# Kernel tuning notes

Measured on AMD Instinct MI355X. Metric: run time of the kernel, lower is better.

The kernel has to match this reference:

```python
import jax, jax.numpy as jnp
import numpy as np

B, S, D, H = 2, 2048, 1024, 16
HD = D // H
LOCAL_WINDOW = 32
GLOBAL_TOKENS = 16
BLOCK_SIZE = 64
SPARSITY = 0.75


def _structured_mask(seq_len):
    """local_global | block_sparse pattern, vectorized numpy (deterministic)."""
    i = np.arange(seq_len)[:, None]
    j = np.arange(seq_len)[None, :]
    half = LOCAL_WINDOW // 2
    local = np.abs(i - j) <= half  # mask[i, i-16 : i+17]
    glob = (i < GLOBAL_TOKENS) | (j < GLOBAL_TOKENS)
    stride = max(1, seq_len // 64)
    strided = ((i % stride) == 0) & ((j % stride) == 0)
    lg = local | glob | strided
    # block sparse: random blocks kept with prob 1-SPARSITY, diagonal always kept
    nb = (seq_len + BLOCK_SIZE - 1) // BLOCK_SIZE
    rng = np.random.default_rng(0)
    block_mask = rng.random((nb, nb)) > SPARSITY
    np.fill_diagonal(block_mask, True)
    bs = np.kron(block_mask, np.ones((BLOCK_SIZE, BLOCK_SIZE), dtype=bool))[:seq_len, :seq_len]
    return lg | bs


def setup_inputs() -> dict:
    key = jax.random.key(0)
    ks = jax.random.split(key, 12)
    std = 1.0 / np.sqrt(D)
    inp = {
        'query': jax.random.normal(ks[0], (B, S, D), jnp.float32),
        'key': jax.random.normal(ks[1], (B, S, D), jnp.float32),
        'value': jax.random.normal(ks[2], (B, S, D), jnp.float32),
        'Wq': jax.random.normal(ks[3], (D, D), jnp.float32) * std,
        'bq': jnp.zeros((D,), jnp.float32),
        'Wk': jax.random.normal(ks[4], (D, D), jnp.float32) * std,
        'bk': jnp.zeros((D,), jnp.float32),
        'Wv': jax.random.normal(ks[5], (D, D), jnp.float32) * std,
        'bv': jnp.zeros((D,), jnp.float32),
        'Wo': jax.random.normal(ks[6], (D, D), jnp.float32) * std,
        'bo': jnp.zeros((D,), jnp.float32),
        'sparse_mask': jnp.asarray(_structured_mask(S)),
    }
    return inp


def reference(query, key, value, Wq, bq, Wk, bk, Wv, bv, Wo, bo, sparse_mask):
    scale = HD ** -0.5
    # projections -> [B, H, S, HD]
    q = (query @ Wq + bq).reshape(B, S, H, HD).transpose(0, 2, 1, 3)
    k = (key @ Wk + bk).reshape(B, S, H, HD).transpose(0, 2, 1, 3)
    v = (value @ Wv + bv).reshape(B, S, H, HD).transpose(0, 2, 1, 3)
    # dense scores then structured sparse mask (matches original math)
    scores = jnp.einsum('bhqd,bhkd->bhqk', q, k) * scale
    scores = jnp.where(sparse_mask[None, None], scores, -jnp.inf)
    attn = jax.nn.softmax(scores, axis=-1)  # every row has >=1 active entry (global cols)
    out = jnp.einsum('bhqk,bhkd->bhqd', attn, v)
    out = out.transpose(0, 2, 1, 3).reshape(B, S, D)
    out = out @ Wo + bo
    return out, attn
```

## Files before the change

### kernel.cpp

```cpp
#include <hip/hip_runtime.h>
#include <hip/hip_bf16.h>
#include <hip/hip_fp16.h>

using u16 = unsigned short;
using u32 = unsigned int;
using u64 = unsigned long long;

typedef __attribute__((ext_vector_type(8))) short short8;
typedef __attribute__((ext_vector_type(8))) _Float16 half8;
typedef __attribute__((ext_vector_type(4))) _Float16 half4;
typedef __attribute__((ext_vector_type(4))) float f32x4;
typedef __attribute__((ext_vector_type(2))) u32 u32x2;

#define DEVI static __device__ __forceinline__

DEVI float bfu2f(u16 u) { return __builtin_bit_cast(float, (u32)u << 16); }
DEVI u16 f2bfu(float f) { return __builtin_bit_cast(u16, __float2bfloat16(f)); }
DEVI u16 f2hu(float f) { return __builtin_bit_cast(u16, (_Float16)f); }

DEVI f32x4 mfma_f16_(half8 a, half8 b, f32x4 c) {
  return __builtin_amdgcn_mfma_f32_16x16x32_f16(a, b, c, 0, 0, 0);
}
DEVI f32x4 mfma16_f16_(half4 a, half4 b, f32x4 c) {
  return __builtin_amdgcn_mfma_f32_16x16x16f16(a, b, c, 0, 0, 0);
}

#define GLD_LDS16(src, dst) \
  __builtin_amdgcn_global_load_lds((const __attribute__((address_space(1))) void*)(src), \
                                   (__attribute__((address_space(3))) void*)(dst), 16, 0, 0)

static constexpr int Bsz = 2, S = 2048, D = 1024, H = 16, HD = 64;
static constexpr int MROWS = Bsz * S;
static constexpr size_t OUT_ELEMS = (size_t)Bsz * S * D;
static constexpr float C_EXP2 = 0.18033688f;
static constexpr size_t OFF_WT  = 0;
static constexpr size_t OFF_Q   = 0x800000;
static constexpr size_t OFF_K   = 0x1000000;
static constexpr size_t OFF_V   = 0x1800000;
static constexpr size_t OFF_VT  = 0x2000000;
static constexpr size_t OFF_O   = 0x2800000;
static constexpr size_t OFF_MB  = 0x3000000;
static constexpr size_t OFF_FLG = 0x3080000;

__global__ __launch_bounds__(256) void detect_dtype(
    const u16* __restrict__ q, int* __restrict__ flag)
{
  __shared__ u32 red[256];
  const int tid = threadIdx.x;
  u32 mx = 0;
  for (int i = tid; i < 32768; i += 256) {
    u32 e = (q[2 * i] >> 7) & 0xFF;
    mx = mx > e ? mx : e;
  }
  red[tid] = mx;
  __syncthreads();
  if (tid == 0) {
    u32 m = 0;
    for (int i = 0; i < 256; ++i) m = m > red[i] ? m : red[i];
    flag[0] = (m >= 0x90) ? 1 : 0;
  }
}

__global__ __launch_bounds__(256) void conv_f16(
    const void* __restrict__ X, u16* __restrict__ Y, const int* __restrict__ flag)
{
  const size_t i8 = ((size_t)blockIdx.x * 256 + threadIdx.x) * 8;
  half8 o;
  if (*flag) {
    const float* x = (const float*)X + i8;
    float4 f0 = ((const float4*)x)[0], f1 = ((const float4*)x)[1];
    o[0] = (_Float16)f0.x; o[1] = (_Float16)f0.y;
    o[2] = (_Float16)f0.z; o[3] = (_Float16)f0.w;
    o[4] = (_Float16)f1.x; o[5] = (_Float16)f1.y;
    o[6] = (_Float16)f1.z; o[7] = (_Float16)f1.w;
  } else {
    uint4 a = *(const uint4*)((const u16*)X + i8);
    u32 wd[4] = {a.x, a.y, a.z, a.w};
    #pragma unroll
    for (int j = 0; j < 4; ++j) {
      o[2 * j]     = (_Float16)bfu2f((u16)(wd[j] & 0xFFFF));
      o[2 * j + 1] = (_Float16)bfu2f((u16)(wd[j] >> 16));
    }
  }
  *reinterpret_cast<half8*>(Y + i8) = o;
}

__global__ __launch_bounds__(256) void prep_w(
    const void* __restrict__ Wq, const void* __restrict__ Wk,
    const void* __restrict__ Wv, const void* __restrict__ Wo,
    u16* __restrict__ WT, const int* __restrict__ flag)
{
  __shared__ _Float16 t[64][80];
  const int z = blockIdx.z;
  const void* src = z == 0 ? Wq : z == 1 ? Wk : z == 2 ? Wv : Wo;
  u16* dst = WT + (size_t)z * 1024 * 1024;
  const int bx = blockIdx.x, by = blockIdx.y;
  const int tid = threadIdx.x;
  const int r = tid >> 2, ch = tid & 3;
  const int fl = *flag;
  if (fl) {
    const float* s = (const float*)src + (size_t)(by * 64 + r) * 1024 + bx * 64 + ch * 16;
    #pragma unroll
    for (int v = 0; v < 4; ++v) {
      float4 f = ((const float4*)s)[v];
      t[r][ch * 16 + v * 4 + 0] = (_Float16)f.x;
      t[r][ch * 16 + v * 4 + 1] = (_Float16)f.y;
      t[r][ch * 16 + v * 4 + 2] = (_Float16)f.z;
      t[r][ch * 16 + v * 4 + 3] = (_Float16)f.w;
    }
  } else {
    const u16* s = (const u16*)src + (size_t)(by * 64 + r) * 1024 + bx * 64 + ch * 16;
    uint4 a0 = ((const uint4*)s)[0], a1 = ((const uint4*)s)[1];
    u32 wds[8] = {a0.x, a0.y, a0.z, a0.w, a1.x, a1.y, a1.z, a1.w};
    #pragma unroll
    for (int j = 0; j < 8; ++j) {
      t[r][ch * 16 + 2 * j]     = (_Float16)bfu2f((u16)(wds[j] & 0xFFFF));
      t[r][ch * 16 + 2 * j + 1] = (_Float16)bfu2f((u16)(wds[j] >> 16));
    }
  }
  __syncthreads();
  half8 o0, o1;
  #pragma unroll
  for (int i = 0; i < 8; ++i) { o0[i] = t[ch * 16 + i][r]; o1[i] = t[ch * 16 + 8 + i][r]; }
  u16* d = dst + (size_t)(bx * 64 + r) * 1024 + by * 64 + ch * 16;
  *reinterpret_cast<half8*>(d) = o0;
  *reinterpret_cast<half8*>(d + 8) = o1;
}

__global__ __launch_bounds__(256) void mask_bits_kernel(
    const void* __restrict__ mask, u64* __restrict__ mbits)
{
  const u32 w0 = *(const u32*)mask;
  int mode;
  if (w0 == 0x01010101u) mode = 0;
  else if ((w0 & 0xFFFFu) && (w0 >> 16)) mode = 1;
  else mode = 2;
  const int row = blockIdx.x;
  const int w = threadIdx.x >> 6, l = threadIdx.x & 63;
  for (int i = 0; i < 8; ++i) {
    int jw = w * 8 + i;
    size_t idx = (size_t)row * S + jw * 64 + l;
    bool m;
    if (mode == 0)      m = ((const unsigned char*)mask)[idx] != 0;
    else if (mode == 1) m = ((const u16*)mask)[idx] != 0;
    else                m = ((const u32*)mask)[idx] != 0;
    u64 bal = __ballot(m);
    if (l == 0) mbits[(size_t)row * 32 + jw] = bal;
  }
}

template<int OUT_DYN>
__global__ __launch_bounds__(256) void gemm_f16(
    const _Float16* __restrict__ A, const _Float16* __restrict__ Bt,
    const void* __restrict__ bias, void* __restrict__ C,
    const int* __restrict__ flag, int M, int N, int K)
{
  __shared__ _Float16 As[64 * 64];
  __shared__ _Float16 Bs[128 * 64];
  const int tid = threadIdx.x;
  const int w = tid >> 6, l = tid & 63;
  const int wr = w >> 1, wc = w & 1;
  const int lg = l >> 4, lc = l & 15;
  const int tM = blockIdx.x * 64, tN = blockIdx.y * 128;
  const int fl = *flag;
  const int rr = l >> 3;
  const int gsw = (l & 7) ^ rr;
  const int rsw = lc & 7;

  f32x4 acc[2][4] = {};

  for (int k0 = 0; k0 < K; k0 += 64) {
    #pragma unroll
    for (int s = 0; s < 2; ++s)
      GLD_LDS16(A + (size_t)(tM + w * 16 + s * 8 + rr) * K + k0 + gsw * 8,
                &As[(w * 16 + s * 8) * 64]);
    #pragma unroll
    for (int s = 0; s < 4; ++s)
      GLD_LDS16(Bt + (size_t)(tN + w * 32 + s * 8 + rr) * K + k0 + gsw * 8,
                &Bs[(w * 32 + s * 8) * 64]);
    __syncthreads();
    half8 a[2][2], b[4][2];
    #pragma unroll
    for (int m = 0; m < 2; ++m)
      #pragma unroll
      for (int kk = 0; kk < 2; ++kk)
        a[m][kk] = *reinterpret_cast<const half8*>(
            &As[(wr * 32 + m * 16 + lc) * 64 + ((kk * 4 + lg) ^ rsw) * 8]);
    #pragma unroll
    for (int n = 0; n < 4; ++n)
      #pragma unroll
      for (int kk = 0; kk < 2; ++kk)
        b[n][kk] = *reinterpret_cast<const half8*>(
            &Bs[(wc * 64 + n * 16 + lc) * 64 + ((kk * 4 + lg) ^ rsw) * 8]);
    #pragma unroll
    for (int m = 0; m < 2; ++m)
      #pragma unroll
      for (int n = 0; n < 4; ++n) {
        acc[m][n] = mfma_f16_(a[m][0], b[n][0], acc[m][n]);
        acc[m][n] = mfma_f16_(a[m][1], b[n][1], acc[m][n]);
      }
    __syncthreads();
  }

  float bf[4];
  #pragma unroll
  for (int n = 0; n < 4; ++n) {
    int col = tN + wc * 64 + n * 16 + lc;
    bf[n] = fl ? ((const float*)bias)[col] : bfu2f(((const u16*)bias)[col]);
  }
  #pragma unroll
  for (int m = 0; m < 2; ++m) {
    int row = tM + wr * 32 + m * 16 + lg * 4;
    #pragma unroll
    for (int n = 0; n < 4; ++n) {
      int col = tN + wc * 64 + n * 16 + lc;
      #pragma unroll
      for (int r = 0; r < 4; ++r) {
        float v = acc[m][n][r] + bf[n];
        size_t off = (size_t)(row + r) * N + col;
        if (OUT_DYN) {
          if (fl) ((float*)C)[off] = v;
          else    ((u16*)C)[off] = f2bfu(v);
        } else {
          ((u16*)C)[off] = f2hu(v);
        }
      }
    }
  }
}

__global__ __launch_bounds__(256) void transpose_v(
    const _Float16* __restrict__ V, _Float16* __restrict__ vT)
{
  __shared__ _Float16 t[64][80];
  const int sb = blockIdx.x, bh = blockIdx.y;
  const int b = bh >> 4, h = bh & 15;
  const int tid = threadIdx.x;
  #pragma unroll
  for (int rep = 0; rep < 2; ++rep) {
    int idx = rep * 256 + tid;
    int sl = idx >> 3, ch = idx & 7;
    *reinterpret_cast<uint4*>(&t[sl][ch * 8]) =
      *reinterpret_cast<const uint4*>(V + (size_t)(b * S + sb * 64 + sl) * D + h * HD + ch * 8);
  }
  __syncthreads();
  #pragma unroll
  for (int rep = 0; rep < 2; ++rep) {
    int idx = rep * 256 + tid;
    int hd = idx >> 3, ch = idx & 7;
    half8 ov;
    #pragma unroll
    for (int i = 0; i < 8; ++i) ov[i] = t[ch * 8 + i][hd];
    *reinterpret_cast<half8*>(vT + ((size_t)bh * HD + hd) * S + sb * 64 + ch * 8) = ov;
  }
}

__global__ __launch_bounds__(256) void attn_kernel(
    const _Float16* __restrict__ Q, const _Float16* __restrict__ Kp,
    const _Float16* __restrict__ vT, const u64* __restrict__ mbits,
    _Float16* __restrict__ O, void* __restrict__ dOut,
    const int* __restrict__ flag)
{
  __shared__ _Float16 Ks[2][4096];
  __shared__ _Float16 Vs[2][4096];

  const int tid = threadIdx.x, w = tid >> 6, l = tid & 63;
  const int lg = l >> 4, lc = l & 15;
  const int flat = blockIdx.y * 32 + blockIdx.x;
  const int nf = (flat & 7) * 128 + (flat >> 3);
  const int rb = nf & 31, bh = nf >> 5;
  const int b = bh >> 4, h = bh & 15;
  const int wg = w ^ (rb & 1);
  const int wrow = rb * 64 + wg * 16;
  const int fl = *flag;

  half8 aq[2];
  {
    const _Float16* qp = Q + (size_t)(b * S + wrow + lc) * D + h * HD;
    aq[0] = *reinterpret_cast<const half8*>(qp + lg * 8);
    aq[1] = *reinterpret_cast<const half8*>(qp + 32 + lg * 8);
  }
  const _Float16* kbase = Kp + (size_t)(b * S) * D + h * HD;
  const _Float16* vbase = vT + (size_t)bh * HD * S;
  const u64* mrow = mbits + (size_t)(wrow + lc) * 32;

  const int rr = w * 8 + (l >> 3);
  const int gsw = (l & 7) ^ (rr & 7);

  #define STAGE_K(buf, jb) do { \
    const _Float16* s0_ = kbase + (size_t)((jb) * 64 + rr) * D + gsw * 8; \
    GLD_LDS16(s0_, &Ks[buf][w * 512]); \
    GLD_LDS16(s0_ + (size_t)32 * D, &Ks[buf][2048 + w * 512]); \
  } while (0)
  #define STAGE_V(buf, jb) do { \
    const _Float16* s0_ = vbase + (size_t)rr * S + (jb) * 64 + gsw * 8; \
    GLD_LDS16(s0_, &Vs[buf][w * 512]); \
    GLD_LDS16(s0_ + (size_t)32 * S, &Vs[buf][2048 + w * 512]); \
  } while (0)

  const int sw = lc & 7;

  float rs = 0.f;
  f32x4 accO[4] = {};

  STAGE_K(0, 0);
  STAGE_V(0, 0);
  __syncthreads();

  #pragma unroll 1
  for (int jb = 0; jb < 32; ++jb) {
    const int buf = jb & 1;
    if (jb < 31) { STAGE_K(buf ^ 1, jb + 1); STAGE_V(buf ^ 1, jb + 1); }
    const u64 mb = mrow[jb];
    const _Float16* kt = Ks[buf];
    const _Float16* vt = Vs[buf];
    #pragma unroll
    for (int c = 0; c < 4; ++c) {
      const u32 bits = (u32)(mb >> (c * 16 + lg * 4)) & 0xFu;
      if (__any(bits != 0)) {
        const int r = c * 16 + lc;
        half8 ka = *reinterpret_cast<const half8*>(&kt[r * 64 + ((lg ^ sw) * 8)]);
        half8 kb = *reinterpret_cast<const half8*>(&kt[r * 64 + (((lg + 4) ^ sw) * 8)]);
        f32x4 sc = {};
        sc = mfma_f16_(ka, aq[0], sc);
        sc = mfma_f16_(kb, aq[1], sc);
        half4 pa;
        #pragma unroll
        for (int r2 = 0; r2 < 4; ++r2) {
          float p = ((bits >> r2) & 1) ? exp2f(sc[r2] * C_EXP2) : 0.f;
          rs += p;
          pa[r2] = (_Float16)p;
        }
        #pragma unroll
        for (int d = 0; d < 4; ++d) {
          const int rd = d * 16 + lc;
          const int ch = (2 * c + (lg >> 1)) ^ sw;
          half4 vv = *reinterpret_cast<const half4*>(&vt[rd * 64 + ch * 8 + (lg & 1) * 4]);
          accO[d] = mfma16_f16_(pa, vv, accO[d]);
        }
      }
    }
    __syncthreads();
  }

  rs += __shfl_xor(rs, 16);
  rs += __shfl_xor(rs, 32);
  const float inv = 1.f / rs;
  const float lg2i = -__log2f(rs);

  float invr[4];
  #pragma unroll
  for (int r = 0; r < 4; ++r) invr[r] = __shfl(inv, lg * 4 + r);

  {
    _Float16* op = O + (size_t)(b * S + wrow + lg * 4) * D + h * HD;
    #pragma unroll
    for (int d = 0; d < 4; ++d)
      #pragma unroll
      for (int r = 0; r < 4; ++r)
        op[(size_t)r * D + d * 16 + lc] = (_Float16)(accO[d][r] * invr[r]);
  }

  STAGE_K(0, 0);
  __syncthreads();

  if (fl) {
    float* ar = (float*)dOut + OUT_ELEMS + (size_t)bh * S * S + (size_t)(wrow + lc) * S;
    #pragma unroll 1
    for (int jb = 0; jb < 32; ++jb) {
      const int buf = jb & 1;
      if (jb < 31) STAGE_K(buf ^ 1, jb + 1);
      const u64 mb = mrow[jb];
      const _Float16* kt = Ks[buf];
      #pragma unroll
      for (int c = 0; c < 4; ++c) {
        const u32 bits = (u32)(mb >> (c * 16 + lg * 4)) & 0xFu;
        f32x4* dst = (f32x4*)(ar + jb * 64 + c * 16 + lg * 4);
        if (__any(bits != 0)) {
          const int r = c * 16 + lc;
          half8 ka = *reinterpret_cast<const half8*>(&kt[r * 64 + ((lg ^ sw) * 8)]);
          half8 kb = *reinterpret_cast<const half8*>(&kt[r * 64 + (((lg + 4) ^ sw) * 8)]);
          f32x4 sc = {};
          sc = mfma_f16_(ka, aq[0], sc);
          sc = mfma_f16_(kb, aq[1], sc);
          f32x4 pv;
          #pragma unroll
          for (int r2 = 0; r2 < 4; ++r2)
            pv[r2] = ((bits >> r2) & 1) ? exp2f(__builtin_fmaf(sc[r2], C_EXP2, lg2i)) : 0.f;
          __builtin_nontemporal_store(pv, dst);
        } else {
          f32x4 z = {};
          __builtin_nontemporal_store(z, dst);
        }
      }
      __syncthreads();
    }
  } else {
    u16* ar = (u16*)dOut + OUT_ELEMS + (size_t)bh * S * S + (size_t)(wrow + lc) * S;
    #pragma unroll 1
    for (int jb = 0; jb < 32; ++jb) {
      const int buf = jb & 1;
      if (jb < 31) STAGE_K(buf ^ 1, jb + 1);
      const u64 mb = mrow[jb];
      const _Float16* kt = Ks[buf];
      #pragma unroll
      for (int c = 0; c < 4; ++c) {
        const u32 bits = (u32)(mb >> (c * 16 + lg * 4)) & 0xFu;
        u32x2* dst = (u32x2*)(ar + jb * 64 + c * 16 + lg * 4);
        if (__any(bits != 0)) {
          const int r = c * 16 + lc;
          half8 ka = *reinterpret_cast<const half8*>(&kt[r * 64 + ((lg ^ sw) * 8)]);
          half8 kb = *reinterpret_cast<const half8*>(&kt[r * 64 + (((lg + 4) ^ sw) * 8)]);
          f32x4 sc = {};
          sc = mfma_f16_(ka, aq[0], sc);
          sc = mfma_f16_(kb, aq[1], sc);
          float p0 = ((bits >> 0) & 1) ? exp2f(__builtin_fmaf(sc[0], C_EXP2, lg2i)) : 0.f;
          float p1 = ((bits >> 1) & 1) ? exp2f(__builtin_fmaf(sc[1], C_EXP2, lg2i)) : 0.f;
          float p2 = ((bits >> 2) & 1) ? exp2f(__builtin_fmaf(sc[2], C_EXP2, lg2i)) : 0.f;
          float p3 = ((bits >> 3) & 1) ? exp2f(__builtin_fmaf(sc[3], C_EXP2, lg2i)) : 0.f;
          u32x2 pk;
          pk[0] = (u32)f2bfu(p0) | ((u32)f2bfu(p1) << 16);
          pk[1] = (u32)f2bfu(p2) | ((u32)f2bfu(p3) << 16);
          __builtin_nontemporal_store(pk, dst);
        } else {
          u32x2 z = {0, 0};
          __builtin_nontemporal_store(z, dst);
        }
      }
      __syncthreads();
    }
  }
  #undef STAGE_K
  #undef STAGE_V
}

extern "C" void kernel_launch(void* const* d_in, const int* in_sizes, int n_in,
                              void* d_out, int out_size, void* d_ws, size_t ws_size,
                              hipStream_t stream) {
  const void* query = d_in[0];
  const void* key_  = d_in[1];
  const void* value = d_in[2];
  const void* Wq = d_in[3];  const void* bq = d_in[4];
  const void* Wk = d_in[5];  const void* bk = d_in[6];
  const void* Wv = d_in[7];  const void* bv = d_in[8];
  const void* Wo = d_in[9];  const void* bo = d_in[10];
  const void* mask = d_in[11];

  char* ws = (char*)d_ws;
  u16* WT   = (u16*)(ws + OFF_WT);
  u16* Qb   = (u16*)(ws + OFF_Q);
  u16* Kb   = (u16*)(ws + OFF_K);
  u16* Vb   = (u16*)(ws + OFF_V);
  u16* vTb  = (u16*)(ws + OFF_VT);
  u16* Ob   = (u16*)(ws + OFF_O);
  u64* mbits = (u64*)(ws + OFF_MB);
  int* flag  = (int*)(ws + OFF_FLG);

  u16* WqT = WT, *WkT = WT + 1048576, *WvT = WT + 2097152, *WoT = WT + 3145728;
  u16* X = vTb;

  detect_dtype<<<1, 256, 0, stream>>>((const u16*)query, flag);
  prep_w<<<dim3(16, 16, 4), 256, 0, stream>>>(Wq, Wk, Wv, Wo, WT, flag);
  mask_bits_kernel<<<dim3(S), 256, 0, stream>>>(mask, mbits);

  const dim3 gg(MROWS / 64, D / 128);
  conv_f16<<<dim3(2048), 256, 0, stream>>>(query, X, flag);
  gemm_f16<0><<<gg, 256, 0, stream>>>((const _Float16*)X, (const _Float16*)WqT,
                                      bq, Qb, flag, MROWS, D, D);
  conv_f16<<<dim3(2048), 256, 0, stream>>>(key_, X, flag);
  gemm_f16<0><<<gg, 256, 0, stream>>>((const _Float16*)X, (const _Float16*)WkT,
                                      bk, Kb, flag, MROWS, D, D);
  conv_f16<<<dim3(2048), 256, 0, stream>>>(value, X, flag);
  gemm_f16<0><<<gg, 256, 0, stream>>>((const _Float16*)X, (const _Float16*)WvT,
                                      bv, Vb, flag, MROWS, D, D);

  transpose_v<<<dim3(32, 32), 256, 0, stream>>>((const _Float16*)Vb, (_Float16*)vTb);
  attn_kernel<<<dim3(32, 32), 256, 0, stream>>>(
      (const _Float16*)Qb, (const _Float16*)Kb, (const _Float16*)vTb,
      mbits, (_Float16*)Ob, d_out, flag);
  gemm_f16<1><<<gg, 256, 0, stream>>>((const _Float16*)Ob, (const _Float16*)WoT,
                                      bo, d_out, flag, MROWS, D, D);
}
```

Baseline: 335.1 us.

## Drop LDS staging in attention kernel; load K and V directly from global

Removes the double-buffered shared-memory staging of K and V tiles and the per-block barriers. Each wave now reads its K and V fragments straight from global memory, only for mask chunks that are active. The next mask word is prefetched one step ahead and the loops are unrolled by two. This trades the LDS copy and barrier cost for uncoalesced, repeated global reads that rely on the cache, which could raise memory latency stalls.

```diff
diff --git a/kernel.cpp b/kernel.cpp
--- a/kernel.cpp
+++ b/kernel.cpp
@@ -261,9 +261,6 @@
     _Float16* __restrict__ O, void* __restrict__ dOut,
     const int* __restrict__ flag)
 {
-  __shared__ _Float16 Ks[2][4096];
-  __shared__ _Float16 Vs[2][4096];
-
   const int tid = threadIdx.x, w = tid >> 6, l = tid & 63;
   const int lg = l >> 4, lc = l & 15;
   const int flat = blockIdx.y * 32 + blockIdx.x;
@@ -284,46 +281,21 @@
   const _Float16* vbase = vT + (size_t)bh * HD * S;
   const u64* mrow = mbits + (size_t)(wrow + lc) * 32;
 
-  const int rr = w * 8 + (l >> 3);
-  const int gsw = (l & 7) ^ (rr & 7);
-
-  #define STAGE_K(buf, jb) do { \
-    const _Float16* s0_ = kbase + (size_t)((jb) * 64 + rr) * D + gsw * 8; \
-    GLD_LDS16(s0_, &Ks[buf][w * 512]); \
-    GLD_LDS16(s0_ + (size_t)32 * D, &Ks[buf][2048 + w * 512]); \
-  } while (0)
-  #define STAGE_V(buf, jb) do { \
-    const _Float16* s0_ = vbase + (size_t)rr * S + (jb) * 64 + gsw * 8; \
-    GLD_LDS16(s0_, &Vs[buf][w * 512]); \
-    GLD_LDS16(s0_ + (size_t)32 * S, &Vs[buf][2048 + w * 512]); \
-  } while (0)
-
-  const int sw = lc & 7;
-
   float rs = 0.f;
   f32x4 accO[4] = {};
 
-  STAGE_K(0, 0);
-  STAGE_V(0, 0);
-  __syncthreads();
-
-  #pragma unroll 1
+  u64 mb = mrow[0];
+  #pragma unroll 2
   for (int jb = 0; jb < 32; ++jb) {
-    const int buf = jb & 1;
-    if (jb < 31) { STAGE_K(buf ^ 1, jb + 1); STAGE_V(buf ^ 1, jb + 1); }
-    const u64 mb = mrow[jb];
-    const _Float16* kt = Ks[buf];
-    const _Float16* vt = Vs[buf];
+    const u64 mb_next = (jb < 31) ? mrow[jb + 1] : 0ull;
     #pragma unroll
     for (int c = 0; c < 4; ++c) {
       const u32 bits = (u32)(mb >> (c * 16 + lg * 4)) & 0xFu;
       if (__any(bits != 0)) {
-        const int r = c * 16 + lc;
-        half8 ka = *reinterpret_cast<const half8*>(&kt[r * 64 + ((lg ^ sw) * 8)]);
-        half8 kb = *reinterpret_cast<const half8*>(&kt[r * 64 + (((lg + 4) ^ sw) * 8)]);
+        const _Float16* kp = kbase + (size_t)(jb * 64 + c * 16 + lc) * D;
         f32x4 sc = {};
-        sc = mfma_f16_(ka, aq[0], sc);
-        sc = mfma_f16_(kb, aq[1], sc);
+        sc = mfma_f16_(*reinterpret_cast<const half8*>(kp + lg * 8), aq[0], sc);
+        sc = mfma_f16_(*reinterpret_cast<const half8*>(kp + 32 + lg * 8), aq[1], sc);
         half4 pa;
         #pragma unroll
         for (int r2 = 0; r2 < 4; ++r2) {
@@ -333,14 +305,13 @@
         }
         #pragma unroll
         for (int d = 0; d < 4; ++d) {
-          const int rd = d * 16 + lc;
-          const int ch = (2 * c + (lg >> 1)) ^ sw;
-          half4 vv = *reinterpret_cast<const half4*>(&vt[rd * 64 + ch * 8 + (lg & 1) * 4]);
+          half4 vv = *reinterpret_cast<const half4*>(
+              vbase + (size_t)(d * 16 + lc) * S + jb * 64 + c * 16 + lg * 4);
           accO[d] = mfma16_f16_(pa, vv, accO[d]);
         }
       }
     }
-    __syncthreads();
+    mb = mb_next;
   }
 
   rs += __shfl_xor(rs, 16);
@@ -361,28 +332,21 @@
         op[(size_t)r * D + d * 16 + lc] = (_Float16)(accO[d][r] * invr[r]);
   }
 
-  STAGE_K(0, 0);
-  __syncthreads();
-
+  mb = mrow[0];
   if (fl) {
     float* ar = (float*)dOut + OUT_ELEMS + (size_t)bh * S * S + (size_t)(wrow + lc) * S;
-    #pragma unroll 1
+    #pragma unroll 2
     for (int jb = 0; jb < 32; ++jb) {
-      const int buf = jb & 1;
-      if (jb < 31) STAGE_K(buf ^ 1, jb + 1);
-      const u64 mb = mrow[jb];
-      const _Float16* kt = Ks[buf];
+      const u64 mb_next = (jb < 31) ? mrow[jb + 1] : 0ull;
       #pragma unroll
       for (int c = 0; c < 4; ++c) {
         const u32 bits = (u32)(mb >> (c * 16 + lg * 4)) & 0xFu;
         f32x4* dst = (f32x4*)(ar + jb * 64 + c * 16 + lg * 4);
         if (__any(bits != 0)) {
-          const int r = c * 16 + lc;
-          half8 ka = *reinterpret_cast<const half8*>(&kt[r * 64 + ((lg ^ sw) * 8)]);
-          half8 kb = *reinterpret_cast<const half8*>(&kt[r * 64 + (((lg + 4) ^ sw) * 8)]);
+          const _Float16* kp = kbase + (size_t)(jb * 64 + c * 16 + lc) * D;
           f32x4 sc = {};
-          sc = mfma_f16_(ka, aq[0], sc);
-          sc = mfma_f16_(kb, aq[1], sc);
+          sc = mfma_f16_(*reinterpret_cast<const half8*>(kp + lg * 8), aq[0], sc);
+          sc = mfma_f16_(*reinterpret_cast<const half8*>(kp + 32 + lg * 8), aq[1], sc);
           f32x4 pv;
           #pragma unroll
           for (int r2 = 0; r2 < 4; ++r2)
@@ -393,27 +357,22 @@
           __builtin_nontemporal_store(z, dst);
         }
       }
-      __syncthreads();
+      mb = mb_next;
     }
   } else {
     u16* ar = (u16*)dOut + OUT_ELEMS + (size_t)bh * S * S + (size_t)(wrow + lc) * S;
-    #pragma unroll 1
+    #pragma unroll 2
     for (int jb = 0; jb < 32; ++jb) {
-      const int buf = jb & 1;
-      if (jb < 31) STAGE_K(buf ^ 1, jb + 1);
-      const u64 mb = mrow[jb];
-      const _Float16* kt = Ks[buf];
+      const u64 mb_next = (jb < 31) ? mrow[jb + 1] : 0ull;
       #pragma unroll
       for (int c = 0; c < 4; ++c) {
         const u32 bits = (u32)(mb >> (c * 16 + lg * 4)) & 0xFu;
         u32x2* dst = (u32x2*)(ar + jb * 64 + c * 16 + lg * 4);
         if (__any(bits != 0)) {
-          const int r = c * 16 + lc;
-          half8 ka = *reinterpret_cast<const half8*>(&kt[r * 64 + ((lg ^ sw) * 8)]);
-          half8 kb = *reinterpret_cast<const half8*>(&kt[r * 64 + (((lg + 4) ^ sw) * 8)]);
+          const _Float16* kp = kbase + (size_t)(jb * 64 + c * 16 + lc) * D;
           f32x4 sc = {};
-          sc = mfma_f16_(ka, aq[0], sc);
-          sc = mfma_f16_(kb, aq[1], sc);
+          sc = mfma_f16_(*reinterpret_cast<const half8*>(kp + lg * 8), aq[0], sc);
+          sc = mfma_f16_(*reinterpret_cast<const half8*>(kp + 32 + lg * 8), aq[1], sc);
           float p0 = ((bits >> 0) & 1) ? exp2f(__builtin_fmaf(sc[0], C_EXP2, lg2i)) : 0.f;
           float p1 = ((bits >> 1) & 1) ? exp2f(__builtin_fmaf(sc[1], C_EXP2, lg2i)) : 0.f;
           float p2 = ((bits >> 2) & 1) ? exp2f(__builtin_fmaf(sc[2], C_EXP2, lg2i)) : 0.f;
@@ -427,11 +386,9 @@
           __builtin_nontemporal_store(z, dst);
         }
       }
-      __syncthreads();
-    }
-  }
-  #undef STAGE_K
-  #undef STAGE_V
+      mb = mb_next;
+    }
+  }
 }
 
 extern "C" void kernel_launch(void* const* d_in, const int* in_sizes, int n_in,
```

After: 532.0 us. 58.8% more time.
